# Kernel optimization log

Measured on AMD Instinct MI355X. Metric: run time of the kernel, lower is better.

Reference implementation:

```python
import jax, jax.numpy as jnp
import numpy as np

E, D, H, K, T = 16, 1024, 2048, 2, 2048


def setup_inputs() -> dict:
    key = jax.random.key(0)
    k = jax.random.split(key, 7)
    scale = 0.02
    return {
        "inp": jax.random.normal(k[0], (T, D), dtype=jnp.float32),
        "gate_idx": jax.random.randint(k[1], (T, K), 0, E, dtype=jnp.int64),
        "gate_score": jax.random.uniform(k[2], (T, K), dtype=jnp.float32),
        "w1": jax.random.normal(k[3], (E, H, D), dtype=jnp.float32) * scale,
        "b1": jnp.zeros((E, H), dtype=jnp.float32),
        "w2": jax.random.normal(k[4], (E, D, H), dtype=jnp.float32) * scale,
        "b2": jnp.zeros((E, D), dtype=jnp.float32),
    }


def reference(inp, gate_idx, gate_score, w1, b1, w2, b2):
    num_expert = w1.shape[0]
    top_k = gate_idx.shape[1]
    d_model = inp.shape[1]
    # expand each token top_k times (repeat_interleave along dim 0)
    x = jnp.repeat(inp, top_k, axis=0)           # [T*K, D]
    g = gate_idx.reshape(-1)                      # [T*K]
    o = jnp.zeros((x.shape[0], d_model), dtype=x.dtype)
    # static loop over experts; output masked by expert assignment (same math
    # as the per-expert gather/scatter in the original)
    for i in range(num_expert):
        h = jax.nn.gelu(x @ w1[i].T + b1[i])      # [T*K, H]
        y = h @ w2[i].T + b2[i]                   # [T*K, D]
        o = o + jnp.where((g == i)[:, None], y, jnp.zeros((), x.dtype))
    # combine top_k expert outputs with gate scores (bmm in the original)
    out = jnp.einsum("nk,nkd->nd", gate_score, o.reshape(-1, top_k, d_model))
    return out
```

## Files before the change

### kernel.cpp

```cpp
#include <hip/hip_runtime.h>
#include <hip/hip_bf16.h>
#include <stdint.h>


#define E_ 16
#define D_ 1024
#define H_ 2048
#define K_ 2
#define T_ 2048
#define NP_ (T_ * K_)
#define MTS_ 48

using short8 = __attribute__((ext_vector_type(8))) short;
using f32x4  = __attribute__((ext_vector_type(4))) float;

__device__ __forceinline__ unsigned short f2bf(float f) {
  union { float f; unsigned u; } x; x.f = f;
  unsigned r = x.u + 0x7fffu + ((x.u >> 16) & 1u);
  return (unsigned short)(r >> 16);
}

__device__ __forceinline__ float gelu_f(float x) {
  float u = 1.5957691216057308f * (x + 0.044715f * x * x * x);
  return x / (1.f + __expf(-u));
}

__device__ __forceinline__ void waitv8() {
  asm volatile("s_waitcnt vmcnt(8)" ::: "memory");
  __builtin_amdgcn_sched_barrier(0);
}
__device__ __forceinline__ void waitv0() {
  asm volatile("s_waitcnt vmcnt(0)" ::: "memory");
  __builtin_amdgcn_sched_barrier(0);
}
__device__ __forceinline__ void barrier_only() {
  __builtin_amdgcn_sched_barrier(0);
  __builtin_amdgcn_s_barrier();
  __builtin_amdgcn_sched_barrier(0);
}
__device__ __forceinline__ void lgkm0_barrier() {
  asm volatile("s_waitcnt lgkmcnt(0)" ::: "memory");
  __builtin_amdgcn_sched_barrier(0);
  __builtin_amdgcn_s_barrier();
  __builtin_amdgcn_sched_barrier(0);
}

__global__ void cvt_kernel(const float* __restrict__ src,
                           unsigned short* __restrict__ dst, int n4) {
  int stride = gridDim.x * blockDim.x;
  for (int i = blockIdx.x * blockDim.x + threadIdx.x; i < n4; i += stride) {
    float4 v = reinterpret_cast<const float4*>(src)[i];
    ushort4 o = make_ushort4(f2bf(v.x), f2bf(v.y), f2bf(v.z), f2bf(v.w));
    reinterpret_cast<ushort4*>(dst)[i] = o;
  }
}

__global__ void route_kernel(const int* __restrict__ gidx,
                             int* __restrict__ rows,
                             int* __restrict__ offsets,
                             int2* __restrict__ tiles) {
  __shared__ int cnt[E_], cur[E_];
  int tid = threadIdx.x;
  if (tid < E_) cnt[tid] = 0;
  __syncthreads();
  for (int p = tid; p < NP_; p += blockDim.x) atomicAdd(&cnt[gidx[p]], 1);
  __syncthreads();
  if (tid == 0) {
    int acc = 0;
    for (int e = 0; e < E_; ++e) { offsets[e] = acc; cur[e] = acc; acc += cnt[e]; }
    offsets[E_] = acc;
    int k = 0;
    for (int e = 0; e < E_; ++e)
      for (int m = offsets[e]; m < offsets[e] + cnt[e]; m += 128)
        tiles[k++] = make_int2(e, m);
    for (; k < MTS_; ++k) tiles[k] = make_int2(-1, 0);
  }
  __syncthreads();
  for (int p = tid; p < NP_; p += blockDim.x) {
    int e = gidx[p];
    int pos = atomicAdd(&cur[e], 1);
    rows[pos] = p;
  }
}

#define GLOAD16(g, l)                                                        \
  __builtin_amdgcn_global_load_lds(                                          \
      (const __attribute__((address_space(1))) unsigned int*)(const void*)(g), \
      (__attribute__((address_space(3))) unsigned int*)(void*)(l), 16, 0, 0)

template<bool IS1>
__global__ __launch_bounds__(256, 3)
void moe_gemm(const unsigned short* __restrict__ A0,
              const float* __restrict__ W,
              const float* __restrict__ bias,
              const int* __restrict__ rows,
              const int* __restrict__ offsets,
              const int2* __restrict__ tiles,
              const float* __restrict__ score,
              unsigned short* __restrict__ Hout,
              float* __restrict__ Yout)
{
  constexpr int BM = 128, BN = 64, BK = 64;
  constexpr int KD = IS1 ? D_ : H_;
  constexpr int NN = IS1 ? H_ : D_;
  constexpr int NT = KD / BK;

  const int2 tile = tiles[blockIdx.y];
  const int e = tile.x;
  if (e < 0) return;
  const int s0   = tile.y;
  const int send = offsets[e + 1];
  const int n0   = blockIdx.x * BN;

  __shared__ unsigned short As[2][BM][BK];
  __shared__ unsigned short Bs[2][BN][BK];
  __shared__ int rowsrc[BM];
  __shared__ int rowdst[BM];

  const int tid  = threadIdx.x;
  const int lane = tid & 63;
  const int wid  = tid >> 6;

  if (tid < BM) {
    int s = s0 + tid;
    bool v = s < send;
    int sc2 = v ? s : s0;
    if (IS1) {
      rowsrc[tid] = rows[sc2] >> 1;
      rowdst[tid] = v ? s : -1;
    } else {
      rowsrc[tid] = sc2;
      rowdst[tid] = v ? rows[s] : -1;
    }
  }
  __syncthreads();

  const int arow  = lane >> 3;
  const int aslot = (lane & 7) ^ arow;
  const unsigned short* gA[4];
#pragma unroll
  for (int i = 0; i < 4; ++i)
    gA[i] = A0 + (size_t)rowsrc[wid * 32 + i * 8 + arow] * KD + aslot * 8;

  const int brow = tid >> 2, bseg = tid & 3;
  const float* gB = W + (size_t)e * NN * KD + (size_t)(n0 + brow) * KD + bseg * 16;

  const int wr = wid >> 1, wc = wid & 1;
  const int fr = lane & 15, fh = lane >> 4;

  f32x4 acc[4][2] = {};
  float4 breg0[4], breg1[4];

  auto issueA = [&](int buf, int kk) {
#pragma unroll
    for (int i = 0; i < 4; ++i)
      GLOAD16(gA[i] + kk, &As[buf][wid * 32 + i * 8][0]);
  };
  auto issueB = [&](float4* br, int kk) {
#pragma unroll
    for (int j = 0; j < 4; ++j)
      br[j] = *reinterpret_cast<const float4*>(gB + kk + j * 4);
  };
  auto writeB = [&](int buf, const float4* br) {
#pragma unroll
    for (int j = 0; j < 2; ++j) {
      short8 v;
#pragma unroll
      for (int q = 0; q < 4; ++q) v[q]     = (short)f2bf((&br[2*j].x)[q]);
#pragma unroll
      for (int q = 0; q < 4; ++q) v[4 + q] = (short)f2bf((&br[2*j+1].x)[q]);
      int slot = (bseg * 2 + j) ^ (brow & 7);
      *reinterpret_cast<short8*>(&Bs[buf][brow][slot * 8]) = v;
    }
  };
  auto compute = [&](int buf) {
    short8 af[4][2], bv[2][2];
#pragma unroll
    for (int mi = 0; mi < 4; ++mi) {
      const int row = wr * 64 + mi * 16 + fr;
#pragma unroll
      for (int ks = 0; ks < 2; ++ks) {
        const int slot = (ks * 4 + fh) ^ (row & 7);
        af[mi][ks] = *reinterpret_cast<const short8*>(&As[buf][row][slot * 8]);
      }
    }
#pragma unroll
    for (int ni = 0; ni < 2; ++ni) {
      const int row = wc * 32 + ni * 16 + fr;
#pragma unroll
      for (int ks = 0; ks < 2; ++ks) {
        const int slot = (ks * 4 + fh) ^ (row & 7);
        bv[ni][ks] = *reinterpret_cast<const short8*>(&Bs[buf][row][slot * 8]);
      }
    }
#pragma unroll
    for (int ks = 0; ks < 2; ++ks)
#pragma unroll
      for (int mi = 0; mi < 4; ++mi)
#pragma unroll
        for (int ni = 0; ni < 2; ++ni)
          acc[mi][ni] = __builtin_amdgcn_mfma_f32_16x16x32_bf16(
              af[mi][ks], bv[ni][ks], acc[mi][ni], 0, 0, 0);
  };

  issueA(0, 0);       issueB(breg0, 0);
  issueA(1, BK);      issueB(breg1, BK);
  waitv8();
  writeB(0, breg0);
  lgkm0_barrier();

  for (int t = 0; t < NT; t += 2) {
    compute(0);
    barrier_only();
    if (t + 2 < NT) {
      issueA(0, (t + 2) * BK); issueB(breg0, (t + 2) * BK);
      waitv8();
    } else {
      waitv0();
    }
    writeB(1, breg1);
    lgkm0_barrier();
    compute(1);
    barrier_only();
    if (t + 2 < NT) {
      if (t + 3 < NT) { issueA(1, (t + 3) * BK); issueB(breg1, (t + 3) * BK); waitv8(); }
      else            { waitv0(); }
      writeB(0, breg0);
      lgkm0_barrier();
    }
  }

  const float* biasE = bias + (size_t)e * NN + n0;
#pragma unroll
  for (int mi = 0; mi < 4; ++mi) {
#pragma unroll
    for (int j = 0; j < 4; ++j) {
      int rt  = wr * 64 + mi * 16 + fh * 4 + j;
      int dst = rowdst[rt];
      if (dst < 0) continue;
      float sc = IS1 ? 0.f : score[dst];
#pragma unroll
      for (int ni = 0; ni < 2; ++ni) {
        int col = wc * 32 + ni * 16 + fr;
        float v = acc[mi][ni][j] + biasE[col];
        if (IS1) {
          Hout[(size_t)dst * H_ + n0 + col] = f2bf(gelu_f(v));
        } else {
          Yout[(size_t)dst * D_ + n0 + col] = v * sc;
        }
      }
    }
  }
}

__global__ void combine_kernel(const float* __restrict__ y,
                               float* __restrict__ out) {
  const int DQ = D_ / 4;
  int i = blockIdx.x * blockDim.x + threadIdx.x;
  int t = i / DQ, d = i % DQ;
  const float4* y4 = reinterpret_cast<const float4*>(y);
  float4 a = y4[(size_t)(2 * t) * DQ + d];
  float4 b = y4[(size_t)(2 * t + 1) * DQ + d];
  reinterpret_cast<float4*>(out)[i] =
      make_float4(a.x + b.x, a.y + b.y, a.z + b.z, a.w + b.w);
}

extern "C" void kernel_launch(void* const* d_in, const int* in_sizes, int n_in,
                              void* d_out, int out_size, void* d_ws, size_t ws_size,
                              hipStream_t stream) {
  const float* inp    = (const float*)d_in[0];
  const int*   gidx   = (const int*)d_in[1];
  const float* gscore = (const float*)d_in[2];
  const float* w1     = (const float*)d_in[3];
  const float* b1     = (const float*)d_in[4];
  const float* w2     = (const float*)d_in[5];
  const float* b2     = (const float*)d_in[6];
  float* out = (float*)d_out;

  char* ws = (char*)d_ws;
  size_t o = 0;
  auto alloc = [&](size_t bytes) {
    void* p = ws + o;
    o = (o + bytes + 255) & ~(size_t)255;
    return p;
  };
  unsigned short* xb   = (unsigned short*)alloc((size_t)T_ * D_ * 2);
  unsigned short* hbuf = (unsigned short*)alloc((size_t)NP_ * H_ * 2);
  float*          ybuf = (float*)alloc((size_t)NP_ * D_ * 4);
  int*            rows = (int*)alloc(NP_ * 4);
  int*         offsets = (int*)alloc((E_ + 1) * 4);
  int2*          tiles = (int2*)alloc(MTS_ * 8);

  cvt_kernel<<<dim3(512), dim3(256), 0, stream>>>(inp, xb, T_ * D_ / 4);
  route_kernel<<<dim3(1), dim3(256), 0, stream>>>(gidx, rows, offsets, tiles);

  moe_gemm<true><<<dim3(H_ / 64, MTS_, 1), dim3(256), 0, stream>>>(
      xb, w1, b1, rows, offsets, tiles, gscore, hbuf, (float*)nullptr);
  moe_gemm<false><<<dim3(D_ / 64, MTS_, 1), dim3(256), 0, stream>>>(
      hbuf, w2, b2, rows, offsets, tiles, gscore, (unsigned short*)nullptr, ybuf);

  combine_kernel<<<dim3(T_ * D_ / 4 / 256), dim3(256), 0, stream>>>(ybuf, out);
}
```

Baseline: 157.1 us.

## Deepen MoE GEMM software pipeline from double to triple buffering

Moves the grouped expert GEMM's global-to-LDS pipeline from two stages to three. A and B tiles are now prefetched three K-steps ahead, with vmcnt waits adjusted to match. The aim is to hide more global-load latency behind MFMA compute. In exchange LDS use and register pressure go up, and launch bounds drop from 3 to 2 blocks per SM, which reduces occupancy.

```diff
diff --git a/kernel.cpp b/kernel.cpp
--- a/kernel.cpp
+++ b/kernel.cpp
@@ -1,6 +1,7 @@
 #include <hip/hip_runtime.h>
 #include <hip/hip_bf16.h>
 #include <stdint.h>
+#include <type_traits>
 
 
 #define E_ 16
@@ -25,6 +26,10 @@
   return x / (1.f + __expf(-u));
 }
 
+__device__ __forceinline__ void waitv16() {
+  asm volatile("s_waitcnt vmcnt(16)" ::: "memory");
+  __builtin_amdgcn_sched_barrier(0);
+}
 __device__ __forceinline__ void waitv8() {
   asm volatile("s_waitcnt vmcnt(8)" ::: "memory");
   __builtin_amdgcn_sched_barrier(0);
@@ -89,7 +94,7 @@
       (__attribute__((address_space(3))) unsigned int*)(void*)(l), 16, 0, 0)
 
 template<bool IS1>
-__global__ __launch_bounds__(256, 3)
+__global__ __launch_bounds__(256, 2)
 void moe_gemm(const unsigned short* __restrict__ A0,
               const float* __restrict__ W,
               const float* __restrict__ bias,
@@ -112,8 +117,8 @@
   const int send = offsets[e + 1];
   const int n0   = blockIdx.x * BN;
 
-  __shared__ unsigned short As[2][BM][BK];
-  __shared__ unsigned short Bs[2][BN][BK];
+  __shared__ unsigned short As[3][BM][BK];
+  __shared__ unsigned short Bs[3][BN][BK];
   __shared__ int rowsrc[BM];
   __shared__ int rowdst[BM];
 
@@ -149,7 +154,8 @@
   const int fr = lane & 15, fh = lane >> 4;
 
   f32x4 acc[4][2] = {};
-  float4 breg0[4], breg1[4];
+  float4 breg0[4], breg1[4], breg2[4];
+  float4* const bregs[3] = {breg0, breg1, breg2};
 
   auto issueA = [&](int buf, int kk) {
 #pragma unroll
@@ -203,31 +209,25 @@
               af[mi][ks], bv[ni][ks], acc[mi][ni], 0, 0, 0);
   };
 
-  issueA(0, 0);       issueB(breg0, 0);
-  issueA(1, BK);      issueB(breg1, BK);
-  waitv8();
-  writeB(0, breg0);
-  lgkm0_barrier();
-
-  for (int t = 0; t < NT; t += 2) {
-    compute(0);
+  issueA(0, 0);        issueB(breg0, 0);
+  issueA(1, BK);       issueB(breg1, BK);
+  issueA(2, 2 * BK);   issueB(breg2, 2 * BK);
+
+  auto body = [&](int t, auto Sc) {
+    constexpr int S = decltype(Sc)::value;
+    if (t + 2 < NT)      waitv16();
+    else if (t + 1 < NT) waitv8();
+    else                 waitv0();
+    writeB(S, bregs[S]);
+    lgkm0_barrier();
+    compute(S);
     barrier_only();
-    if (t + 2 < NT) {
-      issueA(0, (t + 2) * BK); issueB(breg0, (t + 2) * BK);
-      waitv8();
-    } else {
-      waitv0();
-    }
-    writeB(1, breg1);
-    lgkm0_barrier();
-    compute(1);
-    barrier_only();
-    if (t + 2 < NT) {
-      if (t + 3 < NT) { issueA(1, (t + 3) * BK); issueB(breg1, (t + 3) * BK); waitv8(); }
-      else            { waitv0(); }
-      writeB(0, breg0);
-      lgkm0_barrier();
-    }
+    if (t + 3 < NT) { issueA(S, (t + 3) * BK); issueB(bregs[S], (t + 3) * BK); }
+  };
+  for (int t = 0; t < NT; t += 3) {
+    body(t, std::integral_constant<int, 0>{});
+    if (t + 1 < NT) body(t + 1, std::integral_constant<int, 1>{});
+    if (t + 2 < NT) body(t + 2, std::integral_constant<int, 2>{});
   }
 
   const float* biasE = bias + (size_t)e * NN + n0;
@@ -294,9 +294,9 @@
   cvt_kernel<<<dim3(512), dim3(256), 0, stream>>>(inp, xb, T_ * D_ / 4);
   route_kernel<<<dim3(1), dim3(256), 0, stream>>>(gidx, rows, offsets, tiles);
 
-  moe_gemm<true><<<dim3(H_ / 64, MTS_, 1), dim3(256), 0, stream>>>(
+  moe_gemm<true><<<dim3(H_ / 64, MTS_), dim3(256), 0, stream>>>(
       xb, w1, b1, rows, offsets, tiles, gscore, hbuf, (float*)nullptr);
-  moe_gemm<false><<<dim3(D_ / 64, MTS_, 1), dim3(256), 0, stream>>>(
+  moe_gemm<false><<<dim3(D_ / 64, MTS_), dim3(256), 0, stream>>>(
       hbuf, w2, b2, rows, offsets, tiles, gscore, (unsigned short*)nullptr, ybuf);
 
   combine_kernel<<<dim3(T_ * D_ / 4 / 256), dim3(256), 0, stream>>>(ybuf, out);
```

New measurement: 196.3 us. +25.0%, slower.
